# Kernel tuning notes

Measured on AMD Instinct MI355X. Metric: run time of the kernel, lower is better.

## Reference

```python
import jax, jax.numpy as jnp
import numpy as np

HIDDEN = 768
NUM_HEADS = 12
HEAD_DIM = HIDDEN // NUM_HEADS  # 64


def setup_inputs() -> dict:
    key = jax.random.key(0)
    ks = jax.random.split(key, 7)
    B, S = 2, 4096
    scale = 1.0 / np.sqrt(HIDDEN)
    return {
        "hidden_states": jax.random.normal(ks[0], (B, S, HIDDEN), dtype=jnp.float32),
        "Wq": jax.random.normal(ks[1], (HIDDEN, HIDDEN), dtype=jnp.float32) * scale,
        "bq": jnp.zeros((HIDDEN,), dtype=jnp.float32),
        "Wk": jax.random.normal(ks[2], (HIDDEN, HIDDEN), dtype=jnp.float32) * scale,
        "bk": jnp.zeros((HIDDEN,), dtype=jnp.float32),
        "Wv": jax.random.normal(ks[3], (HIDDEN, HIDDEN), dtype=jnp.float32) * scale,
        "bv": jnp.zeros((HIDDEN,), dtype=jnp.float32),
    }


def _split_heads(x):
    # [B, S, H] -> [B, heads, S, head_dim]
    B, S, _ = x.shape
    return x.reshape(B, S, NUM_HEADS, HEAD_DIM).transpose(0, 2, 1, 3)


def reference(hidden_states, Wq, bq, Wk, bk, Wv, bv):
    q = _split_heads(hidden_states @ Wq + bq)  # [B, h, S, d]
    k = _split_heads(hidden_states @ Wk + bk)
    v = _split_heads(hidden_states @ Wv + bv)
    scores = jnp.einsum("bhqd,bhkd->bhqk", q, k) / np.sqrt(HEAD_DIM)
    probs = jax.nn.softmax(scores, axis=-1)  # [B, h, S, S] materialized (eager attn)
    ctx = jnp.einsum("bhqk,bhkd->bhqd", probs, v)
    B, _, S, _ = ctx.shape
    return ctx.transpose(0, 2, 1, 3).reshape(B, S, HIDDEN)
```

## Files before the change

### kernel.cpp

```cpp
#include <hip/hip_runtime.h>
#include <hip/hip_bf16.h>

typedef unsigned short ushort_t;
typedef __attribute__((ext_vector_type(4))) float f32x4;
typedef __attribute__((ext_vector_type(8))) __bf16 bfrag;

#define MFMA16(a,b,c) __builtin_amdgcn_mfma_f32_16x16x32_bf16((a),(b),(c),0,0,0)

#define HID 768
#define NH 12
#define SEQ 4096
#define QSCALE 0.18033688011112042f

#define DRAIN_VMEM() asm volatile("s_waitcnt vmcnt(0)" ::: "memory")

__device__ __forceinline__ unsigned short f2bf(float x) {
  union { float f; unsigned u; } v; v.f = x;
  unsigned r = v.u + 0x7fffu + ((v.u >> 16) & 1u);
  return (unsigned short)(r >> 16);
}

typedef const unsigned char __attribute__((address_space(1)))* gas1_t;
typedef unsigned char __attribute__((address_space(3)))* las3_t;
__device__ __forceinline__ void gload_lds16(const void* g, void* l) {
  __builtin_amdgcn_global_load_lds((gas1_t)(unsigned long long)g,
                                   (las3_t)(unsigned)(unsigned long long)l,
                                   16, 0, 0);
}

__device__ __forceinline__ f32x4 zero4() { f32x4 z = {0.f, 0.f, 0.f, 0.f}; return z; }

__global__ __launch_bounds__(256) void cvt_hidden(const float* __restrict__ hs,
                                                  ushort_t* __restrict__ A) {
  int i = blockIdx.x * 256 + threadIdx.x;
  float4 v = ((const float4*)hs)[i];
  ushort4 o;
  o.x = f2bf(v.x); o.y = f2bf(v.y); o.z = f2bf(v.z); o.w = f2bf(v.w);
  ((ushort4*)A)[i] = o;
}

__global__ __launch_bounds__(256) void transpose_w(const float* __restrict__ Wq,
                                                   const float* __restrict__ Wk,
                                                   const float* __restrict__ Wv,
                                                   ushort_t* __restrict__ Wt) {
  const int z = blockIdx.z;
  const float* W = (z == 0) ? Wq : ((z == 1) ? Wk : Wv);
  const int k0 = blockIdx.x * 64, n0 = blockIdx.y * 64;
  __shared__ float tile[64][65];
  const int t = threadIdx.x;
  const int c4 = (t & 15) * 4;
  const int r = t >> 4;
#pragma unroll
  for (int it = 0; it < 4; ++it) {
    int rr = r + it * 16;
    float4 v = *(const float4*)&W[(size_t)(k0 + rr) * HID + n0 + c4];
    tile[c4 + 0][rr] = v.x; tile[c4 + 1][rr] = v.y;
    tile[c4 + 2][rr] = v.z; tile[c4 + 3][rr] = v.w;
  }
  __syncthreads();
#pragma unroll
  for (int it = 0; it < 4; ++it) {
    int nl = r + it * 16;
    ushort4 o;
    o.x = f2bf(tile[nl][c4 + 0]); o.y = f2bf(tile[nl][c4 + 1]);
    o.z = f2bf(tile[nl][c4 + 2]); o.w = f2bf(tile[nl][c4 + 3]);
    *(ushort4*)&Wt[((size_t)z * HID + n0 + nl) * HID + k0 + c4] = o;
  }
}

__global__ __launch_bounds__(256) void qkv_gemm(const ushort_t* __restrict__ A,
                                                const ushort_t* __restrict__ Wt,
                                                const float* __restrict__ bq,
                                                const float* __restrict__ bk,
                                                const float* __restrict__ bv,
                                                ushort_t* __restrict__ Qh,
                                                ushort_t* __restrict__ Kh,
                                                ushort_t* __restrict__ Vt) {
  __shared__ ushort_t Als[128 * 64];
  __shared__ ushort_t Bls[128 * 64];
  const int z = blockIdx.z;
  const int m0 = blockIdx.x * 128, n0 = blockIdx.y * 128;
  const ushort_t* Wz = Wt + (size_t)z * HID * HID;
  const float* bias = (z == 0) ? bq : ((z == 1) ? bk : bv);
  const int t = threadIdx.x, w = t >> 6, lane = t & 63;
  const int g = lane >> 4, qc = lane & 15;
  const int srow = lane >> 3, sch = lane & 7;
  const int wm = w >> 1, wn = w & 1;

  f32x4 acc[4][4];
#pragma unroll
  for (int mt = 0; mt < 4; ++mt)
#pragma unroll
    for (int nt = 0; nt < 4; ++nt) acc[mt][nt] = zero4();

  for (int kt = 0; kt < 12; ++kt) {
    const int k0 = kt * 64;
#pragma unroll
    for (int i = 0; i < 4; ++i) {
      int row = w * 32 + i * 8 + srow;
      int chA = sch ^ (srow & 7);
      gload_lds16(&A[(size_t)(m0 + row) * HID + k0 + chA * 8],
                  &Als[(w * 32 + i * 8) * 64]);
      gload_lds16(&Wz[(size_t)(n0 + row) * HID + k0 + chA * 8],
                  &Bls[(w * 32 + i * 8) * 64]);
    }
    DRAIN_VMEM();
    __syncthreads();
#pragma unroll
    for (int kk = 0; kk < 2; ++kk) {
      bfrag af[4], bf_[4];
#pragma unroll
      for (int mt = 0; mt < 4; ++mt) {
        int row = wm * 64 + mt * 16 + qc;
        af[mt] = *(const bfrag*)((const char*)Als + row * 128 +
                                 (((kk * 4 + g) ^ (qc & 7)) << 4));
      }
#pragma unroll
      for (int nt = 0; nt < 4; ++nt) {
        int row = wn * 64 + nt * 16 + qc;
        bf_[nt] = *(const bfrag*)((const char*)Bls + row * 128 +
                                  (((kk * 4 + g) ^ (qc & 7)) << 4));
      }
#pragma unroll
      for (int mt = 0; mt < 4; ++mt)
#pragma unroll
        for (int nt = 0; nt < 4; ++nt)
          acc[mt][nt] = MFMA16(af[mt], bf_[nt], acc[mt][nt]);
    }
    __syncthreads();
  }

#pragma unroll
  for (int mt = 0; mt < 4; ++mt) {
#pragma unroll
    for (int nt = 0; nt < 4; ++nt) {
      int n = n0 + wn * 64 + nt * 16 + qc;
      int head = n >> 6, d = n & 63;
      float bb = bias[n];
      int mB = m0 + wm * 64 + mt * 16 + 4 * g;
      int bidx = mB >> 12, s0 = mB & 4095;
      f32x4 a = acc[mt][nt];
      if (z == 2) {
        ushort4 o;
        o.x = f2bf(a[0] + bb); o.y = f2bf(a[1] + bb);
        o.z = f2bf(a[2] + bb); o.w = f2bf(a[3] + bb);
        int scol = (s0 & ~31) | (((s0 >> 2) & 3) << 3) | (((s0 >> 4) & 1) << 2);
        *(ushort4*)&Vt[((size_t)((bidx * NH + head) * 64 + d)) * SEQ + scol] = o;
      } else {
        ushort_t* dst = (z == 0) ? Qh : Kh;
        float sc = (z == 0) ? QSCALE : 1.0f;
        size_t base = (size_t)(bidx * NH + head) * SEQ;
#pragma unroll
        for (int i = 0; i < 4; ++i)
          dst[(base + s0 + i) * 64 + d] = f2bf((a[i] + bb) * sc);
      }
    }
  }
}

__global__ __launch_bounds__(256, 3) void attn_kernel(const ushort_t* __restrict__ Qh,
                                                      const ushort_t* __restrict__ Kh,
                                                      const ushort_t* __restrict__ Vt,
                                                      float* __restrict__ out) {
  const int bh = blockIdx.y;
  const int b = bh / NH, head = bh - b * NH;
  const int t = threadIdx.x, w = t >> 6, lane = t & 63;
  const int g = lane >> 4, qc = lane & 15;
  const ushort_t* Qb = Qh + (size_t)bh * SEQ * 64;
  const ushort_t* Kb = Kh + (size_t)bh * SEQ * 64;
  const ushort_t* Vb = Vt + (size_t)bh * 64 * SEQ;
  const int q0 = blockIdx.x * 128 + w * 32;

  __shared__ ushort_t Kls[2][4096];
  __shared__ ushort_t Vls[2][4096];

  int jr[2], jc[2];
#pragma unroll
  for (int i = 0; i < 2; ++i) {
    int j = w * 128 + i * 64 + lane;
    jr[i] = j >> 3;
    jc[i] = (j & 7) ^ (jr[i] & 7);
  }

  bfrag qv[2][2];
#pragma unroll
  for (int qf = 0; qf < 2; ++qf)
#pragma unroll
    for (int dd = 0; dd < 2; ++dd)
      qv[qf][dd] = *(const bfrag*)&Qb[(size_t)(q0 + qf * 16 + qc) * 64 + dd * 32 + g * 8];

  f32x4 o[2][4];
  f32x4 lacc[2];
#pragma unroll
  for (int qf = 0; qf < 2; ++qf) {
    lacc[qf] = zero4();
#pragma unroll
    for (int dt = 0; dt < 4; ++dt) o[qf][dt] = zero4();
  }
  bfrag ones;
#pragma unroll
  for (int j = 0; j < 8; ++j) ones[j] = (__bf16)1.0f;

#pragma unroll
  for (int i = 0; i < 2; ++i) {
    gload_lds16(&Kb[(size_t)jr[i] * 64 + jc[i] * 8], &Kls[0][(w * 128 + i * 64) * 8]);
    gload_lds16(&Vb[(size_t)jr[i] * SEQ + jc[i] * 8], &Vls[0][(w * 128 + i * 64) * 8]);
  }

  for (int kt = 0; kt < 64; ++kt) {
    const int cur = kt & 1;
    DRAIN_VMEM();
    __syncthreads();
    if (kt < 63) {
      const int kbn = (kt + 1) * 64;
#pragma unroll
      for (int i = 0; i < 2; ++i) {
        gload_lds16(&Kb[(size_t)(kbn + jr[i]) * 64 + jc[i] * 8],
                    &Kls[cur ^ 1][(w * 128 + i * 64) * 8]);
        gload_lds16(&Vb[(size_t)jr[i] * SEQ + kbn + jc[i] * 8],
                    &Vls[cur ^ 1][(w * 128 + i * 64) * 8]);
      }
    }
    const ushort_t* Kc = Kls[cur];
    const ushort_t* Vc = Vls[cur];

    bfrag ak[4][2];
#pragma unroll
    for (int s = 0; s < 4; ++s) {
      const int r = s * 16 + qc;
      ak[s][0] = *(const bfrag*)&Kc[r * 64 + ((g ^ (qc & 7)) * 8)];
      ak[s][1] = *(const bfrag*)&Kc[r * 64 + (((4 + g) ^ (qc & 7)) * 8)];
    }

    bfrag bpq[2][2];
#pragma unroll
    for (int qf = 0; qf < 2; ++qf) {
      f32x4 st[4];
#pragma unroll
      for (int s = 0; s < 4; ++s) {
        f32x4 zz = zero4();
        zz = MFMA16(ak[s][0], qv[qf][0], zz);
        st[s] = MFMA16(ak[s][1], qv[qf][1], zz);
      }
#pragma unroll
      for (int i = 0; i < 4; ++i) {
        bpq[qf][0][i]     = (__bf16)__builtin_amdgcn_exp2f(st[0][i]);
        bpq[qf][0][4 + i] = (__bf16)__builtin_amdgcn_exp2f(st[1][i]);
        bpq[qf][1][i]     = (__bf16)__builtin_amdgcn_exp2f(st[2][i]);
        bpq[qf][1][4 + i] = (__bf16)__builtin_amdgcn_exp2f(st[3][i]);
      }
      lacc[qf] = MFMA16(ones, bpq[qf][0], lacc[qf]);
      lacc[qf] = MFMA16(ones, bpq[qf][1], lacc[qf]);
    }

#pragma unroll
    for (int kk = 0; kk < 2; ++kk) {
#pragma unroll
      for (int dt = 0; dt < 4; ++dt) {
        bfrag av = *(const bfrag*)&Vc[(dt * 16 + qc) * 64 + (((kk * 4 + g) ^ (qc & 7)) * 8)];
        o[0][dt] = MFMA16(av, bpq[0][kk], o[0][dt]);
        o[1][dt] = MFMA16(av, bpq[1][kk], o[1][dt]);
      }
    }
  }

#pragma unroll
  for (int qf = 0; qf < 2; ++qf) {
    float inv = 1.0f / lacc[qf][0];
    int qrow = q0 + qf * 16 + qc;
    float* orow = out + (size_t)(b * SEQ + qrow) * HID + head * 64;
#pragma unroll
    for (int dt = 0; dt < 4; ++dt) {
      float4 vv;
      vv.x = o[qf][dt][0] * inv; vv.y = o[qf][dt][1] * inv;
      vv.z = o[qf][dt][2] * inv; vv.w = o[qf][dt][3] * inv;
      *(float4*)(orow + dt * 16 + 4 * g) = vv;
    }
  }
}

extern "C" void kernel_launch(void* const* d_in, const int* in_sizes, int n_in,
                              void* d_out, int out_size, void* d_ws, size_t ws_size,
                              hipStream_t stream) {
  (void)in_sizes; (void)n_in; (void)out_size; (void)ws_size;
  const float* hs = (const float*)d_in[0];
  const float* Wq = (const float*)d_in[1];
  const float* bq = (const float*)d_in[2];
  const float* Wk = (const float*)d_in[3];
  const float* bk = (const float*)d_in[4];
  const float* Wv = (const float*)d_in[5];
  const float* bv = (const float*)d_in[6];
  float* out = (float*)d_out;

  char* ws = (char*)d_ws;
  ushort_t* Abf = (ushort_t*)ws;
  ushort_t* Wt  = (ushort_t*)(ws + 12582912);
  ushort_t* Qh  = (ushort_t*)(ws + 12582912 + 3538944);
  ushort_t* Kh  = Qh + 6291456;
  ushort_t* Vt  = Kh + 6291456;

  cvt_hidden<<<6144, 256, 0, stream>>>(hs, Abf);
  transpose_w<<<dim3(12, 12, 3), 256, 0, stream>>>(Wq, Wk, Wv, Wt);
  qkv_gemm<<<dim3(64, 6, 3), 256, 0, stream>>>(Abf, Wt, bq, bk, bv, Qh, Kh, Vt);
  attn_kernel<<<dim3(32, 24), 256, 0, stream>>>(Qh, Kh, Vt, out);
}
```

Baseline: 164.8 us.

## Split key tiles across warp pairs in attention and reduce partials via LDS

Each block now covers 64 queries instead of 128. The four warps form two query halves times two key halves: each warp handles 32 queries against half of every 64-key tile. Partial outputs and row sums from the second key-half warps go through reused LDS and are summed before normalization. This doubles the grid from 768 to 1536 blocks to improve occupancy and load balance across CUs. The cost is that each K/V tile is loaded for half as many queries, which doubles global K/V traffic, and an LDS reduction is added at the end.

```diff
diff --git a/kernel.cpp b/kernel.cpp
--- a/kernel.cpp
+++ b/kernel.cpp
@@ -166,10 +166,11 @@
   const int b = bh / NH, head = bh - b * NH;
   const int t = threadIdx.x, w = t >> 6, lane = t & 63;
   const int g = lane >> 4, qc = lane & 15;
+  const int qh = w >> 1, kh = w & 1;
   const ushort_t* Qb = Qh + (size_t)bh * SEQ * 64;
   const ushort_t* Kb = Kh + (size_t)bh * SEQ * 64;
   const ushort_t* Vb = Vt + (size_t)bh * 64 * SEQ;
-  const int q0 = blockIdx.x * 128 + w * 32;
+  const int q0 = blockIdx.x * 64 + qh * 32;
 
   __shared__ ushort_t Kls[2][4096];
   __shared__ ushort_t Vls[2][4096];
@@ -224,57 +225,73 @@
     const ushort_t* Kc = Kls[cur];
     const ushort_t* Vc = Vls[cur];
 
-    bfrag ak[4][2];
-#pragma unroll
-    for (int s = 0; s < 4; ++s) {
-      const int r = s * 16 + qc;
+    bfrag ak[2][2];
+#pragma unroll
+    for (int s = 0; s < 2; ++s) {
+      const int r = kh * 32 + s * 16 + qc;
       ak[s][0] = *(const bfrag*)&Kc[r * 64 + ((g ^ (qc & 7)) * 8)];
       ak[s][1] = *(const bfrag*)&Kc[r * 64 + (((4 + g) ^ (qc & 7)) * 8)];
     }
-
-    bfrag bpq[2][2];
+    bfrag av[4];
+#pragma unroll
+    for (int dt = 0; dt < 4; ++dt)
+      av[dt] = *(const bfrag*)&Vc[(dt * 16 + qc) * 64 + (((kh * 4 + g) ^ (qc & 7)) * 8)];
+
+    bfrag bpq[2];
 #pragma unroll
     for (int qf = 0; qf < 2; ++qf) {
-      f32x4 st[4];
-#pragma unroll
-      for (int s = 0; s < 4; ++s) {
+      f32x4 st[2];
+#pragma unroll
+      for (int s = 0; s < 2; ++s) {
         f32x4 zz = zero4();
         zz = MFMA16(ak[s][0], qv[qf][0], zz);
         st[s] = MFMA16(ak[s][1], qv[qf][1], zz);
       }
+      bfrag p;
 #pragma unroll
       for (int i = 0; i < 4; ++i) {
-        bpq[qf][0][i]     = (__bf16)__builtin_amdgcn_exp2f(st[0][i]);
-        bpq[qf][0][4 + i] = (__bf16)__builtin_amdgcn_exp2f(st[1][i]);
-        bpq[qf][1][i]     = (__bf16)__builtin_amdgcn_exp2f(st[2][i]);
-        bpq[qf][1][4 + i] = (__bf16)__builtin_amdgcn_exp2f(st[3][i]);
-      }
-      lacc[qf] = MFMA16(ones, bpq[qf][0], lacc[qf]);
-      lacc[qf] = MFMA16(ones, bpq[qf][1], lacc[qf]);
-    }
-
-#pragma unroll
-    for (int kk = 0; kk < 2; ++kk) {
+        p[i]     = (__bf16)__builtin_amdgcn_exp2f(st[0][i]);
+        p[4 + i] = (__bf16)__builtin_amdgcn_exp2f(st[1][i]);
+      }
+      bpq[qf] = p;
+      lacc[qf] = MFMA16(ones, p, lacc[qf]);
+    }
+
+#pragma unroll
+    for (int dt = 0; dt < 4; ++dt) {
+      o[0][dt] = MFMA16(av[dt], bpq[0], o[0][dt]);
+      o[1][dt] = MFMA16(av[dt], bpq[1], o[1][dt]);
+    }
+  }
+
+  __syncthreads();
+  float* redO = (float*)&Kls[0][0];
+  float* redL = (float*)&Vls[0][0];
+  if (kh == 1) {
+#pragma unroll
+    for (int qf = 0; qf < 2; ++qf) {
+#pragma unroll
+      for (int dt = 0; dt < 4; ++dt)
+        *(f32x4*)&redO[qh * 2048 + (qf * 4 + dt) * 256 + lane * 4] = o[qf][dt];
+      redL[qh * 128 + qf * 64 + lane] = lacc[qf][0];
+    }
+  }
+  __syncthreads();
+  if (kh == 0) {
+#pragma unroll
+    for (int qf = 0; qf < 2; ++qf) {
+      float l = lacc[qf][0] + redL[qh * 128 + qf * 64 + lane];
+      float inv = 1.0f / l;
+      int qrow = q0 + qf * 16 + qc;
+      float* orow = out + (size_t)(b * SEQ + qrow) * HID + head * 64;
 #pragma unroll
       for (int dt = 0; dt < 4; ++dt) {
-        bfrag av = *(const bfrag*)&Vc[(dt * 16 + qc) * 64 + (((kk * 4 + g) ^ (qc & 7)) * 8)];
-        o[0][dt] = MFMA16(av, bpq[0][kk], o[0][dt]);
-        o[1][dt] = MFMA16(av, bpq[1][kk], o[1][dt]);
-      }
-    }
-  }
-
-#pragma unroll
-  for (int qf = 0; qf < 2; ++qf) {
-    float inv = 1.0f / lacc[qf][0];
-    int qrow = q0 + qf * 16 + qc;
-    float* orow = out + (size_t)(b * SEQ + qrow) * HID + head * 64;
-#pragma unroll
-    for (int dt = 0; dt < 4; ++dt) {
-      float4 vv;
-      vv.x = o[qf][dt][0] * inv; vv.y = o[qf][dt][1] * inv;
-      vv.z = o[qf][dt][2] * inv; vv.w = o[qf][dt][3] * inv;
-      *(float4*)(orow + dt * 16 + 4 * g) = vv;
+        f32x4 p = *(f32x4*)&redO[qh * 2048 + (qf * 4 + dt) * 256 + lane * 4];
+        f32x4 s = o[qf][dt] + p;
+        float4 vv;
+        vv.x = s[0] * inv; vv.y = s[1] * inv; vv.z = s[2] * inv; vv.w = s[3] * inv;
+        *(float4*)(orow + dt * 16 + 4 * g) = vv;
+      }
     }
   }
 }
@@ -302,5 +319,5 @@
   cvt_hidden<<<6144, 256, 0, stream>>>(hs, Abf);
   transpose_w<<<dim3(12, 12, 3), 256, 0, stream>>>(Wq, Wk, Wv, Wt);
   qkv_gemm<<<dim3(64, 6, 3), 256, 0, stream>>>(Abf, Wt, bq, bk, bv, Qh, Kh, Vt);
-  attn_kernel<<<dim3(32, 24), 256, 0, stream>>>(Qh, Kh, Vt, out);
-}
+  attn_kernel<<<dim3(64, 24), 256, 0, stream>>>(Qh, Kh, Vt, out);
+}
```

Result: slower. 174.4 us (+5.9%).

## Triple-buffer K/V tiles in attention with partial vmcnt waits and MFMA priority

Applied to the files above, without the earlier changes.

The attention kernel moves from double to triple buffering of K/V LDS tiles, prefetching two tiles ahead and waiting only until the older tile's loads land (vmcnt(4)) instead of draining all outstanding loads each iteration. It also raises wave priority around the MFMA blocks with s_setprio so matrix work is issued ahead of other waves. The aim is to hide global-to-LDS latency behind compute. In exchange, LDS use grows from 32KB to 48KB per block, which may reduce occupancy against the launch-bounds target of 3 blocks per CU.

```diff
diff --git a/kernel.cpp b/kernel.cpp
--- a/kernel.cpp
+++ b/kernel.cpp
@@ -12,7 +12,8 @@
 #define SEQ 4096
 #define QSCALE 0.18033688011112042f
 
-#define DRAIN_VMEM() asm volatile("s_waitcnt vmcnt(0)" ::: "memory")
+#define WAIT_VMCNT0() asm volatile("s_waitcnt vmcnt(0)" ::: "memory")
+#define WAIT_VMCNT4() asm volatile("s_waitcnt vmcnt(4)" ::: "memory")
 
 __device__ __forceinline__ unsigned short f2bf(float x) {
   union { float f; unsigned u; } v; v.f = x;
@@ -104,7 +105,7 @@
       gload_lds16(&Wz[(size_t)(n0 + row) * HID + k0 + chA * 8],
                   &Bls[(w * 32 + i * 8) * 64]);
     }
-    DRAIN_VMEM();
+    WAIT_VMCNT0();
     __syncthreads();
 #pragma unroll
     for (int kk = 0; kk < 2; ++kk) {
@@ -171,8 +172,8 @@
   const ushort_t* Vb = Vt + (size_t)bh * 64 * SEQ;
   const int q0 = blockIdx.x * 128 + w * 32;
 
-  __shared__ ushort_t Kls[2][4096];
-  __shared__ ushort_t Vls[2][4096];
+  __shared__ ushort_t Kls[3][4096];
+  __shared__ ushort_t Vls[3][4096];
 
   int jr[2], jc[2];
 #pragma unroll
@@ -202,23 +203,31 @@
   for (int j = 0; j < 8; ++j) ones[j] = (__bf16)1.0f;
 
 #pragma unroll
-  for (int i = 0; i < 2; ++i) {
-    gload_lds16(&Kb[(size_t)jr[i] * 64 + jc[i] * 8], &Kls[0][(w * 128 + i * 64) * 8]);
-    gload_lds16(&Vb[(size_t)jr[i] * SEQ + jc[i] * 8], &Vls[0][(w * 128 + i * 64) * 8]);
-  }
-
+  for (int tt = 0; tt < 2; ++tt) {
+    const int kb = tt * 64;
+#pragma unroll
+    for (int i = 0; i < 2; ++i) {
+      gload_lds16(&Kb[(size_t)(kb + jr[i]) * 64 + jc[i] * 8],
+                  &Kls[tt][(w * 128 + i * 64) * 8]);
+      gload_lds16(&Vb[(size_t)jr[i] * SEQ + kb + jc[i] * 8],
+                  &Vls[tt][(w * 128 + i * 64) * 8]);
+    }
+  }
+
+  int cur = 0;
   for (int kt = 0; kt < 64; ++kt) {
-    const int cur = kt & 1;
-    DRAIN_VMEM();
+    if (kt < 63) WAIT_VMCNT4();
+    else         WAIT_VMCNT0();
     __syncthreads();
-    if (kt < 63) {
-      const int kbn = (kt + 1) * 64;
+    if (kt < 62) {
+      const int sbuf = (cur >= 1) ? cur - 1 : cur + 2;
+      const int kbn = (kt + 2) * 64;
 #pragma unroll
       for (int i = 0; i < 2; ++i) {
         gload_lds16(&Kb[(size_t)(kbn + jr[i]) * 64 + jc[i] * 8],
-                    &Kls[cur ^ 1][(w * 128 + i * 64) * 8]);
+                    &Kls[sbuf][(w * 128 + i * 64) * 8]);
         gload_lds16(&Vb[(size_t)jr[i] * SEQ + kbn + jc[i] * 8],
-                    &Vls[cur ^ 1][(w * 128 + i * 64) * 8]);
+                    &Vls[sbuf][(w * 128 + i * 64) * 8]);
       }
     }
     const ushort_t* Kc = Kls[cur];
@@ -236,12 +245,14 @@
 #pragma unroll
     for (int qf = 0; qf < 2; ++qf) {
       f32x4 st[4];
+      __builtin_amdgcn_s_setprio(1);
 #pragma unroll
       for (int s = 0; s < 4; ++s) {
         f32x4 zz = zero4();
         zz = MFMA16(ak[s][0], qv[qf][0], zz);
         st[s] = MFMA16(ak[s][1], qv[qf][1], zz);
       }
+      __builtin_amdgcn_s_setprio(0);
 #pragma unroll
       for (int i = 0; i < 4; ++i) {
         bpq[qf][0][i]     = (__bf16)__builtin_amdgcn_exp2f(st[0][i]);
@@ -253,6 +264,7 @@
       lacc[qf] = MFMA16(ones, bpq[qf][1], lacc[qf]);
     }
 
+    __builtin_amdgcn_s_setprio(1);
 #pragma unroll
     for (int kk = 0; kk < 2; ++kk) {
 #pragma unroll
@@ -262,6 +274,9 @@
         o[1][dt] = MFMA16(av, bpq[1][kk], o[1][dt]);
       }
     }
+    __builtin_amdgcn_s_setprio(0);
+
+    cur = (cur == 2) ? 0 : cur + 1;
   }
 
 #pragma unroll
```

New measurement: 167.1 us. Within noise of the previous version (+1.4%).
